# Kernel tuning notes

Hardware: AMD Instinct MI355X
Metric: run time of the kernel (lower is better)

The kernel has to match this reference:

```python
import jax, jax.numpy as jnp
import numpy as np

NUM_HEADS = 5
TEMP = 0.3
NEG_FILL = -1e-7  # note: NOT -inf; masked entries still contribute ~exp(0) to softmax, faithful to torch code


def setup_inputs() -> dict:
    key = jax.random.key(0)
    k1, k2, k3, k4, k5 = jax.random.split(key, 5)
    B, N, F_IN, F_OUT = 8, 1024, 320, 320
    h = jax.random.normal(k1, (B, N, F_IN), dtype=jnp.float32)
    Wqk = jax.random.normal(k2, (F_IN, 2 * F_IN), dtype=jnp.float32) * (1.0 / np.sqrt(F_IN))
    bqk = jax.random.normal(k3, (2 * F_IN,), dtype=jnp.float32) * 0.01
    weight = jax.random.normal(k4, (F_IN, F_OUT), dtype=jnp.float32) * (1.0 / np.sqrt(F_OUT))
    bias = jax.random.normal(k5, (F_OUT,), dtype=jnp.float32) * 0.01
    return {"h": h, "Wqk": Wqk, "bqk": bqk, "weight": weight, "bias": bias}


def reference(h, Wqk, bqk, weight, bias):
    B, N, F = h.shape
    H = NUM_HEADS
    D = F // H
    # linear -> [b, n, 2F]; einops 'b n (h d qk)' => reshape (b, n, h, d, 2)
    qk = (h @ Wqk + bqk).reshape(B, N, H, D, 2)
    q = jnp.transpose(qk[..., 0], (0, 2, 1, 3))  # b h n d
    k = jnp.transpose(qk[..., 1], (0, 2, 1, 3))  # b h n d
    scale = D ** -0.5
    dots = jnp.einsum('bhqd,bhkd->bhqk', q, k) * scale  # b h n n
    at = dots.sum(axis=1)  # b n n  (sum over heads)
    # sort-based threshold: keep values >= descending-sorted value at index N//6
    thr = jax.lax.top_k(at, N // 6 + 1)[0][..., -1]  # b n
    adj = jnp.where(at < thr[:, :, None], jnp.asarray(NEG_FILL, at.dtype), at)
    attn = jax.nn.softmax(adj / TEMP, axis=2)  # b n n
    out_feature = jnp.einsum('bij,bjd->bid', attn, h)  # values = raw input h
    return out_feature @ weight + bias
```

## Files before the change

### kernel.cpp

```cpp
#include <hip/hip_runtime.h>
#include <hip/hip_fp16.h>


typedef __attribute__((ext_vector_type(8))) _Float16 half8;
typedef __attribute__((ext_vector_type(4))) float f32x4;

#define WAITV(N) do { asm volatile("s_waitcnt vmcnt(" #N ")" ::: "memory"); \
                      __builtin_amdgcn_sched_barrier(0); } while (0)

__device__ __forceinline__ void stage_tile(const __half* g, __half* lds,
                                           int nrow16, int ld, int wave, int lane) {
    const int r = lane >> 2;
    const int c = ((lane & 3) ^ ((lane >> 3) & 3)) * 8;
    for (int i = wave; i < nrow16; i += 4) {
        const __half* src = g + (long)(i * 16 + r) * ld + c;
        __builtin_amdgcn_global_load_lds(
            (const __attribute__((address_space(1))) unsigned int*)src,
            (__attribute__((address_space(3))) unsigned int*)(lds + i * 512),
            16, 0, 0);
    }
}

__device__ __forceinline__ void stage_wave(const __half* g, __half* lds,
                                           int nrow16, int ld, int lane) {
    const int r = lane >> 2;
    const int c = ((lane & 3) ^ ((lane >> 3) & 3)) * 8;
    for (int i = 0; i < nrow16; ++i) {
        const __half* src = g + (long)(i * 16 + r) * ld + c;
        __builtin_amdgcn_global_load_lds(
            (const __attribute__((address_space(1))) unsigned int*)src,
            (__attribute__((address_space(3))) unsigned int*)(lds + i * 512),
            16, 0, 0);
    }
}

template <int EPI>
__device__ __forceinline__ void gemm_body(
    const __half* __restrict__ A, const __half* __restrict__ B,
    void* __restrict__ C, void* __restrict__ C2, const float* __restrict__ bias,
    int lda, int ldb, int ldc, int bx, int by, __half* smem)
{
    constexpr int BUF = 16384;
    const int tid  = threadIdx.x;
    const int lane = tid & 63;
    const int wave = tid >> 6;
    const int wm   = wave >> 1;
    const int wn   = wave & 1;

    const __half* Ab = A + (long)by * 128 * lda;
    const __half* Bb = B + (long)bx * 128 * ldb;

    f32x4 acc[4][4];
    #pragma unroll
    for (int i = 0; i < 4; ++i)
        #pragma unroll
        for (int j = 0; j < 4; ++j) acc[i][j] = (f32x4){0.f, 0.f, 0.f, 0.f};

    const int lrow = lane & 15;
    const int quad = lane >> 4;
    const int swz = (quad ^ ((lrow >> 1) & 3)) * 8;

    #pragma unroll
    for (int c = 0; c < 2; ++c) {
        stage_tile(Ab + c * 32, smem + c * 4096, 8, lda, wave, lane);
        stage_tile(Bb + c * 32, smem + 8192 + c * 4096, 8, ldb, wave, lane);
    }

    for (int it = 0; it < 5; ++it) {
        __syncthreads();
        if (it + 1 < 5) {
            __half* nb = smem + ((it + 1) & 1) * BUF;
            const int k1 = (it + 1) * 64;
            #pragma unroll
            for (int c = 0; c < 2; ++c) {
                stage_tile(Ab + k1 + c * 32, nb + c * 4096, 8, lda, wave, lane);
                stage_tile(Bb + k1 + c * 32, nb + 8192 + c * 4096, 8, ldb, wave, lane);
            }
        }
        const __half* buf = smem + (it & 1) * BUF;
        #pragma unroll
        for (int c = 0; c < 2; ++c) {
            const __half* pA = buf + c * 4096 + (wm * 64 + lrow) * 32 + swz;
            const __half* pB = buf + 8192 + c * 4096 + (wn * 64 + lrow) * 32 + swz;
            half8 ah[4], bh[4];
            #pragma unroll
            for (int mt = 0; mt < 4; ++mt) ah[mt] = *(const half8*)(pA + mt * 512);
            #pragma unroll
            for (int nt = 0; nt < 4; ++nt) bh[nt] = *(const half8*)(pB + nt * 512);
            #pragma unroll
            for (int mt = 0; mt < 4; ++mt)
                #pragma unroll
                for (int nt = 0; nt < 4; ++nt)
                    acc[mt][nt] = __builtin_amdgcn_mfma_f32_16x16x32_f16(
                        ah[mt], bh[nt], acc[mt][nt], 0, 0, 0);
        }
    }

    const int row_base = by * 128 + wm * 64;
    const int col_base = bx * 128 + wn * 64;
    #pragma unroll
    for (int mt = 0; mt < 4; ++mt)
        #pragma unroll
        for (int nt = 0; nt < 4; ++nt)
            #pragma unroll
            for (int r = 0; r < 4; ++r) {
                const int row = row_base + mt * 16 + quad * 4 + r;
                const int col = col_base + nt * 16 + lrow;
                const float v = acc[mt][nt][r];
                if (EPI == 1) {
                    const float val = v + bias[col];
                    const long idx = (long)row * 320 + (col >> 1);
                    if (col & 1) ((__half*)C2)[idx] = __float2half(val);
                    else         ((__half*)C)[idx]  = __float2half(val);
                } else {
                    ((__half*)C)[(long)row * ldc + col] = __float2half(v);
                }
            }
}

__global__ __launch_bounds__(256) void g1_combined(
    const __half* __restrict__ h16, const __half* __restrict__ wTp,
    const __half* __restrict__ WqkT, __half* __restrict__ hWT,
    __half* __restrict__ Q, __half* __restrict__ Kb,
    const float* __restrict__ bqk)
{
    __shared__ __half smem[2 * 16384];
    const int bx = blockIdx.x;
    if (bx < 192) {
        gemm_body<2>(wTp, h16, hWT, nullptr, nullptr,
                     320, 320, 8192, bx % 64, bx / 64, smem);
    } else {
        const int b = bx - 192;
        gemm_body<1>(h16, WqkT, Q, Kb, bqk,
                     320, 320, 320, b % 5, b / 5, smem);
    }
}

__global__ __launch_bounds__(256) void prep_all(
    const float* __restrict__ h, ushort4* __restrict__ h16,
    const float* __restrict__ Wqk, __half* __restrict__ WqkT,
    const float* __restrict__ weight, __half* __restrict__ wTp)
{
    const int bx = blockIdx.x;
    if (bx < 2560) {
        const int i = bx * 256 + threadIdx.x;
        const float4 v = ((const float4*)h)[i];
        ushort4 o;
        o.x = __half_as_ushort(__float2half(v.x));
        o.y = __half_as_ushort(__float2half(v.y));
        o.z = __half_as_ushort(__float2half(v.z));
        o.w = __half_as_ushort(__float2half(v.w));
        h16[i] = o;
        return;
    }
    __shared__ float t[32][33];
    const float* src;
    __half* dst;
    int ldS, ldT, c0, r0;
    if (bx < 2760) {
        const int b = bx - 2560;
        src = Wqk; dst = WqkT; ldS = 640; ldT = 320;
        c0 = (b % 20) * 32; r0 = (b / 20) * 32;
    } else {
        const int b = bx - 2760;
        src = weight; dst = wTp; ldS = 320; ldT = 320;
        c0 = (b % 10) * 32; r0 = (b / 10) * 32;
    }
    const int lx = threadIdx.x & 31, ly = threadIdx.x >> 5;
    #pragma unroll
    for (int i = 0; i < 4; ++i)
        t[ly + 8 * i][lx] = src[(long)(r0 + ly + 8 * i) * ldS + c0 + lx];
    __syncthreads();
    #pragma unroll
    for (int i = 0; i < 4; ++i)
        dst[(long)(c0 + ly + 8 * i) * ldT + r0 + lx] = __float2half(t[lx][ly + 8 * i]);
}

__global__ __launch_bounds__(512, 2) void fused_attn(
    const __half* __restrict__ Q, const __half* __restrict__ Kmat,
    const __half* __restrict__ hWT, const float* __restrict__ bias,
    float* __restrict__ out)
{
    __shared__ __half smem[77824];
    __half* const P  = smem;
    __half* const S  = smem + 32768;
    __half* const QL = S;
    __half* const KB = S + 10240;
    __half* const WB = S;
    int (*const hist)[256] = (int(*)[256])(smem + 73728);

    const int tid  = threadIdx.x;
    const int lane = tid & 63;
    const int wave = tid >> 6;
    const int lrow = lane & 15;
    const int quad = lane >> 4;
    const int swz  = (quad ^ ((lrow >> 1) & 3)) * 8;

    const int b  = blockIdx.x & 7;
    const int r0 = (blockIdx.x >> 3) * 32;

    const __half* Qb = Q    + (long)(b * 1024 + r0) * 320;
    const __half* Kb = Kmat + (long)b * 327680;
    const __half* Wb = hWT  + (long)b * 1024;

    for (int i = wave; i < 20; i += 8) {
        const int s   = i * 64 + lane;
        const int row = s / 40;
        const int cb  = s % 40;
        const int gb  = cb ^ (row & 7);
        const __half* src = Qb + (long)row * 320 + gb * 8;
        __builtin_amdgcn_global_load_lds(
            (const __attribute__((address_space(1))) unsigned int*)src,
            (__attribute__((address_space(3))) unsigned int*)(QL + i * 512),
            16, 0, 0);
    }
    __half* const kb0 = KB + wave * 4096;
    stage_wave(Kb + (long)(wave * 128) * 320, kb0, 4, 320, lane);
    __syncthreads();

    #pragma unroll
    for (int cg = 0; cg < 2; ++cg) {
        f32x4 acc[4][2];
        #pragma unroll
        for (int i = 0; i < 4; ++i)
            #pragma unroll
            for (int j = 0; j < 2; ++j) acc[i][j] = (f32x4){0.f, 0.f, 0.f, 0.f};

        for (int kc = 0; kc < 10; ++kc) {
            const int r = cg * 10 + kc;
            if (r + 1 < 20) {
                const int cg1 = (r + 1) / 10, kc1 = (r + 1) % 10;
                stage_wave(Kb + (long)(wave * 128 + cg1 * 64) * 320 + kc1 * 32,
                           kb0 + ((r + 1) & 1) * 2048, 4, 320, lane);
                WAITV(4);
            } else {
                WAITV(0);
            }
            const __half* kt = kb0 + (r & 1) * 2048;
            const int gbq = kc * 4 + quad;
            half8 ah[2], bh[4];
            #pragma unroll
            for (int mi = 0; mi < 2; ++mi)
                ah[mi] = *(const half8*)&QL[(mi * 16 + lrow) * 320
                                            + (gbq ^ (lrow & 7)) * 8];
            #pragma unroll
            for (int cb = 0; cb < 4; ++cb)
                bh[cb] = *(const half8*)(kt + (cb * 16 + lrow) * 32 + swz);
            #pragma unroll
            for (int cb = 0; cb < 4; ++cb)
                #pragma unroll
                for (int mi = 0; mi < 2; ++mi)
                    acc[cb][mi] = __builtin_amdgcn_mfma_f32_16x16x32_f16(
                        ah[mi], bh[cb], acc[cb][mi], 0, 0, 0);
        }
        #pragma unroll
        for (int cb = 0; cb < 4; ++cb)
            #pragma unroll
            for (int mi = 0; mi < 2; ++mi)
                #pragma unroll
                for (int rr = 0; rr < 4; ++rr) {
                    const int row = mi * 16 + quad * 4 + rr;
                    const int col = wave * 128 + cg * 64 + cb * 16 + lrow;
                    P[((row << 10) + col) ^ ((row & 7) << 3)] =
                        __float2half(0.125f * acc[cb][mi][rr]);
                }
    }
    __syncthreads();

    const int q4 = wave & 3;
    const int kh = wave >> 2;
    __half* const wb0 = WB + wave * 5120;
    const __half* Wbase = Wb + (long)(q4 * 80) * 8192 + kh * 512;
    stage_wave(Wbase, wb0, 5, 8192, lane);

    #pragma unroll
    for (int j = 0; j < 4; ++j) {
        const int row  = wave * 4 + j;
        const int key8 = (row & 7) << 3;
        const int base = (row << 10) + lane * 16;

        unsigned short vs[16];
        *(uint4*)&vs[0] = *(const uint4*)&P[base ^ key8];
        *(uint4*)&vs[8] = *(const uint4*)&P[(base + 8) ^ key8];

        unsigned key[16];
        #pragma unroll
        for (int i = 0; i < 16; ++i) {
            const unsigned u = vs[i];
            key[i] = (u & 0x8000u) ? ((~u) & 0xFFFFu) : (u | 0x8000u);
        }

        unsigned prefix = 0, pmask = 0;
        int kk = 171;

        #pragma unroll
        for (int pass = 0; pass < 2; ++pass) {
            const int shift = 8 - 8 * pass;
            *(int4*)&hist[wave][lane * 4] = make_int4(0, 0, 0, 0);
            #pragma unroll
            for (int i = 0; i < 16; ++i) {
                if ((key[i] & pmask) == prefix)
                    atomicAdd(&hist[wave][(key[i] >> shift) & 255], 1);
            }
            const int4 hh = *(const int4*)&hist[wave][lane * 4];
            const int s = hh.x + hh.y + hh.z + hh.w;
            int suf = s;
            #pragma unroll
            for (int off = 1; off < 64; off <<= 1) {
                const int o = __shfl_down(suf, off);
                if (lane + off < 64) suf += o;
            }
            const int cgt3 = suf - s;
            const int cgt2 = cgt3 + hh.w;
            const int cgt1 = cgt2 + hh.z;
            const int cgt0 = cgt1 + hh.y;
            int pick = 0x7FFFFFFF;
            if (cgt3 < kk && kk <= cgt3 + hh.w) pick = ((4 * lane + 3) << 16) | (kk - cgt3);
            if (cgt2 < kk && kk <= cgt2 + hh.z) pick = ((4 * lane + 2) << 16) | (kk - cgt2);
            if (cgt1 < kk && kk <= cgt1 + hh.y) pick = ((4 * lane + 1) << 16) | (kk - cgt1);
            if (cgt0 < kk && kk <= cgt0 + hh.x) pick = ((4 * lane + 0) << 16) | (kk - cgt0);
            #pragma unroll
            for (int off = 32; off > 0; off >>= 1) pick = min(pick, __shfl_xor(pick, off));
            const unsigned digit = (unsigned)(pick >> 16);
            kk = pick & 0xFFFF;
            prefix |= digit << shift;
            pmask  |= 0xFFu << shift;
        }

        const unsigned short tu = (prefix & 0x8000u) ? (unsigned short)(prefix & 0x7FFFu)
                                                     : (unsigned short)((~prefix) & 0xFFFFu);
        const float thr = __half2float(__ushort_as_half(tu));

        float lg[16];
        float mx = -3.4e38f;
        #pragma unroll
        for (int i = 0; i < 16; ++i) {
            const float v = __half2float(__ushort_as_half(vs[i]));
            const float a = (v < thr) ? -1e-7f : v;
            lg[i] = a * (1.0f / 0.3f);
            mx = fmaxf(mx, lg[i]);
        }
        #pragma unroll
        for (int off = 32; off > 0; off >>= 1) mx = fmaxf(mx, __shfl_xor(mx, off));

        float e[16];
        float sum = 0.f;
        #pragma unroll
        for (int i = 0; i < 16; ++i) { e[i] = __expf(lg[i] - mx); sum += e[i]; }
        #pragma unroll
        for (int off = 32; off > 0; off >>= 1) sum += __shfl_xor(sum, off);
        const float inv = 1.0f / sum;

        unsigned short os[16];
        #pragma unroll
        for (int i = 0; i < 16; ++i) os[i] = __half_as_ushort(__float2half(e[i] * inv));
        *(uint4*)&P[base ^ key8]       = *(const uint4*)&os[0];
        *(uint4*)&P[(base + 8) ^ key8] = *(const uint4*)&os[8];
    }
    __syncthreads();

    f32x4 acc4[5][2];
    #pragma unroll
    for (int i = 0; i < 5; ++i)
        #pragma unroll
        for (int j = 0; j < 2; ++j) acc4[i][j] = (f32x4){0.f, 0.f, 0.f, 0.f};

    for (int t = 0; t < 16; ++t) {
        if (t + 1 < 16) {
            stage_wave(Wbase + (t + 1) * 32, wb0 + ((t + 1) & 1) * 2560,
                       5, 8192, lane);
            WAITV(5);
        } else {
            WAITV(0);
        }
        const __half* T = wb0 + (t & 1) * 2560;
        const int kk = kh * 512 + t * 32 + quad * 8;
        half8 ah[2], bh[5];
        #pragma unroll
        for (int mi = 0; mi < 2; ++mi) {
            const int row = mi * 16 + lrow;
            ah[mi] = *(const half8*)&P[((row << 10) + kk) ^ ((row & 7) << 3)];
        }
        #pragma unroll
        for (int cf = 0; cf < 5; ++cf)
            bh[cf] = *(const half8*)(T + (cf * 16 + lrow) * 32 + swz);
        #pragma unroll
        for (int cf = 0; cf < 5; ++cf)
            #pragma unroll
            for (int mi = 0; mi < 2; ++mi)
                acc4[cf][mi] = __builtin_amdgcn_mfma_f32_16x16x32_f16(
                    ah[mi], bh[cf], acc4[cf][mi], 0, 0, 0);
    }

    __syncthreads();
    float* const red = (float*)P;
    if (kh == 1) {
        #pragma unroll
        for (int cf = 0; cf < 5; ++cf)
            #pragma unroll
            for (int mi = 0; mi < 2; ++mi)
                #pragma unroll
                for (int rr = 0; rr < 4; ++rr)
                    red[(mi * 16 + quad * 4 + rr) * 320 + q4 * 80 + cf * 16 + lrow] =
                        acc4[cf][mi][rr];
    }
    __syncthreads();
    if (kh == 0) {
        #pragma unroll
        for (int cf = 0; cf < 5; ++cf)
            #pragma unroll
            for (int mi = 0; mi < 2; ++mi)
                #pragma unroll
                for (int rr = 0; rr < 4; ++rr) {
                    const int row = mi * 16 + quad * 4 + rr;
                    const int col = q4 * 80 + cf * 16 + lrow;
                    out[(long)(b * 1024 + r0 + row) * 320 + col] =
                        acc4[cf][mi][rr] + red[row * 320 + col] + bias[col];
                }
    }
}

extern "C" void kernel_launch(void* const* d_in, const int* in_sizes, int n_in,
                              void* d_out, int out_size, void* d_ws, size_t ws_size,
                              hipStream_t stream) {
    (void)in_sizes; (void)n_in; (void)out_size; (void)ws_size;

    const float* h      = (const float*)d_in[0];
    const float* Wqk    = (const float*)d_in[1];
    const float* bqk    = (const float*)d_in[2];
    const float* weight = (const float*)d_in[3];
    const float* bias   = (const float*)d_in[4];
    float* out = (float*)d_out;

    char* p = (char*)d_ws;
    __half* h16  = (__half*)p; p += 2621440L * 2;
    __half* Q    = (__half*)p; p += 2621440L * 2;
    __half* Kb   = (__half*)p; p += 2621440L * 2;
    __half* WqkT = (__half*)p; p += 640L * 320 * 2;
    __half* wTp  = (__half*)p; p += 384L * 320 * 2;
    __half* hWT  = (__half*)p; p += 384L * 8192 * 2;

    prep_all<<<2860, 256, 0, stream>>>(h, (ushort4*)h16, Wqk, WqkT, weight, wTp);

    g1_combined<<<512, 256, 0, stream>>>(h16, wTp, WqkT, hWT, Q, Kb, bqk);

    fused_attn<<<256, 512, 0, stream>>>(Q, Kb, hWT, bias, out);
}
```

Measured before the change: 126.0 us.

## Replace block-tiled projection GEMM with independent per-wave 64x64 tiles

The first GEMM stage moves from 128x128 block tiles (four waves sharing LDS, synchronized with __syncthreads) to independent 64x64 tiles, one per wave. Each wave double-buffers its own LDS slice and waits with s_waitcnt vmcnt instead of block barriers. This raises the number of work units (1920 wave tiles over 480 blocks versus 512 blocks) and removes barrier stalls. The cost is less operand reuse per loaded tile, so global and LDS traffic goes up.

```diff
diff --git a/kernel.cpp b/kernel.cpp
--- a/kernel.cpp
+++ b/kernel.cpp
@@ -7,19 +7,6 @@
 
 #define WAITV(N) do { asm volatile("s_waitcnt vmcnt(" #N ")" ::: "memory"); \
                       __builtin_amdgcn_sched_barrier(0); } while (0)
-
-__device__ __forceinline__ void stage_tile(const __half* g, __half* lds,
-                                           int nrow16, int ld, int wave, int lane) {
-    const int r = lane >> 2;
-    const int c = ((lane & 3) ^ ((lane >> 3) & 3)) * 8;
-    for (int i = wave; i < nrow16; i += 4) {
-        const __half* src = g + (long)(i * 16 + r) * ld + c;
-        __builtin_amdgcn_global_load_lds(
-            (const __attribute__((address_space(1))) unsigned int*)src,
-            (__attribute__((address_space(3))) unsigned int*)(lds + i * 512),
-            16, 0, 0);
-    }
-}
 
 __device__ __forceinline__ void stage_wave(const __half* g, __half* lds,
                                            int nrow16, int ld, int lane) {
@@ -31,108 +18,6 @@
             (const __attribute__((address_space(1))) unsigned int*)src,
             (__attribute__((address_space(3))) unsigned int*)(lds + i * 512),
             16, 0, 0);
-    }
-}
-
-template <int EPI>
-__device__ __forceinline__ void gemm_body(
-    const __half* __restrict__ A, const __half* __restrict__ B,
-    void* __restrict__ C, void* __restrict__ C2, const float* __restrict__ bias,
-    int lda, int ldb, int ldc, int bx, int by, __half* smem)
-{
-    constexpr int BUF = 16384;
-    const int tid  = threadIdx.x;
-    const int lane = tid & 63;
-    const int wave = tid >> 6;
-    const int wm   = wave >> 1;
-    const int wn   = wave & 1;
-
-    const __half* Ab = A + (long)by * 128 * lda;
-    const __half* Bb = B + (long)bx * 128 * ldb;
-
-    f32x4 acc[4][4];
-    #pragma unroll
-    for (int i = 0; i < 4; ++i)
-        #pragma unroll
-        for (int j = 0; j < 4; ++j) acc[i][j] = (f32x4){0.f, 0.f, 0.f, 0.f};
-
-    const int lrow = lane & 15;
-    const int quad = lane >> 4;
-    const int swz = (quad ^ ((lrow >> 1) & 3)) * 8;
-
-    #pragma unroll
-    for (int c = 0; c < 2; ++c) {
-        stage_tile(Ab + c * 32, smem + c * 4096, 8, lda, wave, lane);
-        stage_tile(Bb + c * 32, smem + 8192 + c * 4096, 8, ldb, wave, lane);
-    }
-
-    for (int it = 0; it < 5; ++it) {
-        __syncthreads();
-        if (it + 1 < 5) {
-            __half* nb = smem + ((it + 1) & 1) * BUF;
-            const int k1 = (it + 1) * 64;
-            #pragma unroll
-            for (int c = 0; c < 2; ++c) {
-                stage_tile(Ab + k1 + c * 32, nb + c * 4096, 8, lda, wave, lane);
-                stage_tile(Bb + k1 + c * 32, nb + 8192 + c * 4096, 8, ldb, wave, lane);
-            }
-        }
-        const __half* buf = smem + (it & 1) * BUF;
-        #pragma unroll
-        for (int c = 0; c < 2; ++c) {
-            const __half* pA = buf + c * 4096 + (wm * 64 + lrow) * 32 + swz;
-            const __half* pB = buf + 8192 + c * 4096 + (wn * 64 + lrow) * 32 + swz;
-            half8 ah[4], bh[4];
-            #pragma unroll
-            for (int mt = 0; mt < 4; ++mt) ah[mt] = *(const half8*)(pA + mt * 512);
-            #pragma unroll
-            for (int nt = 0; nt < 4; ++nt) bh[nt] = *(const half8*)(pB + nt * 512);
-            #pragma unroll
-            for (int mt = 0; mt < 4; ++mt)
-                #pragma unroll
-                for (int nt = 0; nt < 4; ++nt)
-                    acc[mt][nt] = __builtin_amdgcn_mfma_f32_16x16x32_f16(
-                        ah[mt], bh[nt], acc[mt][nt], 0, 0, 0);
-        }
-    }
-
-    const int row_base = by * 128 + wm * 64;
-    const int col_base = bx * 128 + wn * 64;
-    #pragma unroll
-    for (int mt = 0; mt < 4; ++mt)
-        #pragma unroll
-        for (int nt = 0; nt < 4; ++nt)
-            #pragma unroll
-            for (int r = 0; r < 4; ++r) {
-                const int row = row_base + mt * 16 + quad * 4 + r;
-                const int col = col_base + nt * 16 + lrow;
-                const float v = acc[mt][nt][r];
-                if (EPI == 1) {
-                    const float val = v + bias[col];
-                    const long idx = (long)row * 320 + (col >> 1);
-                    if (col & 1) ((__half*)C2)[idx] = __float2half(val);
-                    else         ((__half*)C)[idx]  = __float2half(val);
-                } else {
-                    ((__half*)C)[(long)row * ldc + col] = __float2half(v);
-                }
-            }
-}
-
-__global__ __launch_bounds__(256) void g1_combined(
-    const __half* __restrict__ h16, const __half* __restrict__ wTp,
-    const __half* __restrict__ WqkT, __half* __restrict__ hWT,
-    __half* __restrict__ Q, __half* __restrict__ Kb,
-    const float* __restrict__ bqk)
-{
-    __shared__ __half smem[2 * 16384];
-    const int bx = blockIdx.x;
-    if (bx < 192) {
-        gemm_body<2>(wTp, h16, hWT, nullptr, nullptr,
-                     320, 320, 8192, bx % 64, bx / 64, smem);
-    } else {
-        const int b = bx - 192;
-        gemm_body<1>(h16, WqkT, Q, Kb, bqk,
-                     320, 320, 320, b % 5, b / 5, smem);
     }
 }
 
@@ -176,6 +61,100 @@
         dst[(long)(c0 + ly + 8 * i) * ldT + r0 + lx] = __float2half(t[lx][ly + 8 * i]);
 }
 
+__global__ __launch_bounds__(256) void g1_wave(
+    const __half* __restrict__ h16, const __half* __restrict__ wTp,
+    const __half* __restrict__ WqkT, __half* __restrict__ hWT,
+    __half* __restrict__ Qo, __half* __restrict__ Ko,
+    const float* __restrict__ bqk)
+{
+    __shared__ __half smem[32768];
+    const int tid  = threadIdx.x;
+    const int lane = tid & 63;
+    const int wave = tid >> 6;
+    const int lrow = lane & 15;
+    const int quad = lane >> 4;
+    const int swz  = (quad ^ ((lrow >> 1) & 3)) * 8;
+
+    __half* const ab = smem + wave * 8192;
+    __half* const bb = smem + wave * 8192 + 4096;
+
+    const int gid = blockIdx.x * 4 + wave;
+    const __half *Aw, *Bw;
+    int row_base, col_base, epi;
+    if (gid < 640) {
+        const int m = gid % 5, n = gid / 5;
+        Aw = wTp + (long)m * 64 * 320;
+        Bw = h16 + (long)n * 64 * 320;
+        row_base = m * 64; col_base = n * 64; epi = 2;
+    } else {
+        const int g2 = gid - 640;
+        const int r = g2 % 128, c = g2 / 128;
+        Aw = h16  + (long)r * 64 * 320;
+        Bw = WqkT + (long)c * 64 * 320;
+        row_base = r * 64; col_base = c * 64; epi = 1;
+    }
+
+    f32x4 acc[4][4];
+    #pragma unroll
+    for (int i = 0; i < 4; ++i)
+        #pragma unroll
+        for (int j = 0; j < 4; ++j) acc[i][j] = (f32x4){0.f, 0.f, 0.f, 0.f};
+
+    stage_wave(Aw, ab, 4, 320, lane);
+    stage_wave(Bw, bb, 4, 320, lane);
+
+    #pragma unroll
+    for (int kc = 0; kc < 10; ++kc) {
+        if (kc < 9) {
+            stage_wave(Aw + (kc + 1) * 32, ab + ((kc + 1) & 1) * 2048, 4, 320, lane);
+            stage_wave(Bw + (kc + 1) * 32, bb + ((kc + 1) & 1) * 2048, 4, 320, lane);
+            WAITV(8);
+        } else {
+            WAITV(0);
+        }
+        const __half* pa = ab + (kc & 1) * 2048;
+        const __half* pb = bb + (kc & 1) * 2048;
+        half8 ah[4], bh[4];
+        #pragma unroll
+        for (int mt = 0; mt < 4; ++mt) ah[mt] = *(const half8*)(pa + (mt * 16 + lrow) * 32 + swz);
+        #pragma unroll
+        for (int nt = 0; nt < 4; ++nt) bh[nt] = *(const half8*)(pb + (nt * 16 + lrow) * 32 + swz);
+        #pragma unroll
+        for (int mt = 0; mt < 4; ++mt)
+            #pragma unroll
+            for (int nt = 0; nt < 4; ++nt)
+                acc[mt][nt] = __builtin_amdgcn_mfma_f32_16x16x32_f16(
+                    ah[mt], bh[nt], acc[mt][nt], 0, 0, 0);
+    }
+
+    if (epi == 2) {
+        #pragma unroll
+        for (int mt = 0; mt < 4; ++mt)
+            #pragma unroll
+            for (int nt = 0; nt < 4; ++nt)
+                #pragma unroll
+                for (int r = 0; r < 4; ++r) {
+                    const int row = row_base + mt * 16 + quad * 4 + r;
+                    const int col = col_base + nt * 16 + lrow;
+                    hWT[(long)row * 8192 + col] = __float2half(acc[mt][nt][r]);
+                }
+    } else {
+        #pragma unroll
+        for (int mt = 0; mt < 4; ++mt)
+            #pragma unroll
+            for (int nt = 0; nt < 4; ++nt)
+                #pragma unroll
+                for (int r = 0; r < 4; ++r) {
+                    const int row = row_base + mt * 16 + quad * 4 + r;
+                    const int col = col_base + nt * 16 + lrow;
+                    const float val = acc[mt][nt][r] + bqk[col];
+                    const long idx = (long)row * 320 + (col >> 1);
+                    if (col & 1) Ko[idx] = __float2half(val);
+                    else         Qo[idx] = __float2half(val);
+                }
+    }
+}
+
 __global__ __launch_bounds__(512, 2) void fused_attn(
     const __half* __restrict__ Q, const __half* __restrict__ Kmat,
     const __half* __restrict__ hWT, const float* __restrict__ bias,
@@ -442,7 +421,7 @@
 
     prep_all<<<2860, 256, 0, stream>>>(h, (ushort4*)h16, Wqk, WqkT, weight, wTp);
 
-    g1_combined<<<512, 256, 0, stream>>>(h16, wTp, WqkT, hWT, Q, Kb, bqk);
+    g1_wave<<<480, 256, 0, stream>>>(h16, wTp, WqkT, hWT, Q, Kb, bqk);
 
     fused_attn<<<256, 512, 0, stream>>>(Q, Kb, hWT, bias, out);
 }
```

After: 127.2 us (median of 2 runs). No clear change (+1.0%).
